# Performance work log

Measured on AMD Instinct MI355X. Metric: run time of the kernel, lower is better.

## Reference

```python
import jax, jax.numpy as jnp
import numpy as np

SS = 25.0 / 255.0   # spatial_scale = 1 / (SEARCH_SIZE/25), SEARCH_SIZE = 255
OUT = 7             # ROIPOOL_OUTSIZE // 4, ROIPOOL_OUTSIZE = 28
SP = 4              # sample_per_part (mmdet DeformRoIPooling default)
TRANS_STD = 0.1


def _deform_roi_pool(x, rois, offset):
    # x: [B,C,H,W]; rois: [N,5] (batch_idx,x1,y1,x2,y2); offset: [N,2,OUT,OUT] (ch0=x, ch1=y)
    B, C, H, W = x.shape
    N = rois.shape[0]
    b = rois[:, 0].astype(jnp.int32)
    sw = jnp.round(rois[:, 1]) * SS - 0.5
    sh = jnp.round(rois[:, 2]) * SS - 0.5
    rw = jnp.maximum((jnp.round(rois[:, 3]) + 1.0) * SS - 0.5 - sw, 0.1)
    rh = jnp.maximum((jnp.round(rois[:, 4]) + 1.0) * SS - 0.5 - sh, 0.1)
    bw, bh = rw / OUT, rh / OUT
    p = jnp.arange(OUT, dtype=x.dtype)
    tx = offset[:, 0] * TRANS_STD  # [N,OUT,OUT] indexed [n,ph,pw]
    ty = offset[:, 1] * TRANS_STD
    wstart = p[None, None, :] * bw[:, None, None] + sw[:, None, None] + tx * rw[:, None, None]
    hstart = p[None, :, None] * bh[:, None, None] + sh[:, None, None] + ty * rh[:, None, None]
    s = jnp.arange(SP, dtype=x.dtype)
    # sample coords [N,OUT,OUT,SP(ih),SP(iw)]
    sx = wstart[..., None, None] + s[None, None, None, None, :] * (bw / SP)[:, None, None, None, None]
    sy = hstart[..., None, None] + s[None, None, None, :, None] * (bh / SP)[:, None, None, None, None]
    valid = (sx >= -0.5) & (sx <= W - 0.5) & (sy >= -0.5) & (sy <= H - 0.5)
    xc = jnp.clip(sx, 0.0, W - 1.0)
    yc = jnp.clip(sy, 0.0, H - 1.0)
    x0 = jnp.floor(xc)
    y0 = jnp.floor(yc)
    dx = xc - x0
    dy = yc - y0
    xi0 = x0.astype(jnp.int32)
    yi0 = y0.astype(jnp.int32)
    xi1 = jnp.ceil(xc).astype(jnp.int32)
    yi1 = jnp.ceil(yc).astype(jnp.int32)
    feat = jnp.transpose(x, (0, 2, 3, 1))  # [B,H,W,C]
    bb = b[:, None, None, None, None]

    def g(yi, xi):
        return feat[bb, yi, xi]  # [N,OUT,OUT,SP,SP,C]

    val = (((1 - dx) * (1 - dy))[..., None] * g(yi0, xi0)
           + (dx * (1 - dy))[..., None] * g(yi0, xi1)
           + ((1 - dx) * dy)[..., None] * g(yi1, xi0)
           + (dx * dy)[..., None] * g(yi1, xi1))
    val = jnp.where(valid[..., None], val, 0.0)
    cnt = valid.sum(axis=(3, 4)).astype(x.dtype)              # [N,OUT,OUT]
    pooled = val.sum(axis=(3, 4)) / jnp.maximum(cnt, 1.0)[..., None]
    return jnp.transpose(pooled, (0, 3, 1, 2))                # [N,C,OUT,OUT]


def _lin(h, w, b):
    return h @ w.T + b


def _forward(x, rois, off_w1, off_b1, off_w2, off_b2, off_w3, off_b3,
             fc1_w, fc1_b, fc2_w, fc2_b, box_w, box_b):
    N = rois.shape[0]
    zero_off = jnp.zeros((N, 2, OUT, OUT), x.dtype)
    # pass 1: no-trans pooling -> offset prediction
    p0 = _deform_roi_pool(x, rois, zero_off).reshape(N, -1)
    h = jax.nn.relu(_lin(p0, off_w1, off_b1))
    h = jax.nn.relu(_lin(h, off_w2, off_b2))
    off = _lin(h, off_w3, off_b3).reshape(N, 2, OUT, OUT)
    # pass 2: deformable pooling with predicted offsets
    p = _deform_roi_pool(x, rois, off).reshape(N, -1)
    h = jax.nn.relu(_lin(p, fc1_w, fc1_b))
    h = jax.nn.relu(_lin(h, fc2_w, fc2_b))
    return _lin(h, box_w, box_b)  # [N,4]


def setup_inputs():
    key = jax.random.key(0)
    ks = jax.random.split(key, 16)
    B, C, H, W, N = 8, 256, 25, 25, 256
    IN = C * OUT * OUT  # 12544
    DFC, FCC = 1024, 512
    x = jax.random.normal(ks[0], (B, C, H, W), jnp.float32)
    bidx = jax.random.randint(ks[1], (N,), 0, B).astype(jnp.float32)
    x1 = jax.random.uniform(ks[2], (N,), minval=0.0, maxval=180.0)
    y1 = jax.random.uniform(ks[3], (N,), minval=0.0, maxval=180.0)
    wd = jax.random.uniform(ks[4], (N,), minval=24.0, maxval=120.0)
    ht = jax.random.uniform(ks[5], (N,), minval=24.0, maxval=120.0)
    rois = jnp.stack([bidx, x1, y1, jnp.clip(x1 + wd, 0.0, 254.0),
                      jnp.clip(y1 + ht, 0.0, 254.0)], axis=1)

    def lin_p(k, o, i):
        return jax.random.normal(k, (o, i), jnp.float32) * (1.0 / np.sqrt(i))

    return dict(
        x=x, rois=rois,
        off_w1=lin_p(ks[6], DFC, IN), off_b1=jnp.zeros((DFC,), jnp.float32),
        off_w2=lin_p(ks[7], DFC, DFC), off_b2=jnp.zeros((DFC,), jnp.float32),
        off_w3=lin_p(ks[8], 2 * OUT * OUT, DFC) * 0.1,
        off_b3=jnp.zeros((2 * OUT * OUT,), jnp.float32),
        fc1_w=lin_p(ks[9], FCC, IN), fc1_b=jnp.zeros((FCC,), jnp.float32),
        fc2_w=lin_p(ks[10], FCC, FCC), fc2_b=jnp.zeros((FCC,), jnp.float32),
        box_w=lin_p(ks[11], 4, FCC) * 0.001, box_b=jnp.zeros((4,), jnp.float32),
    )


def reference(x, rois, off_w1, off_b1, off_w2, off_b2, off_w3, off_b3,
              fc1_w, fc1_b, fc2_w, fc2_b, box_w, box_b):
    return _forward(x, rois, off_w1, off_b1, off_w2, off_b2, off_w3, off_b3,
                    fc1_w, fc1_b, fc2_w, fc2_b, box_w, box_b)
```

## Files before the change

### kernel.cpp

```cpp
#include <hip/hip_runtime.h>
#include <hip/hip_bf16.h>


#define NROI 256
#define NB   8
#define INF  12544
#define DFC  1024
#define FCC  512

typedef __attribute__((ext_vector_type(8))) short short8;
typedef __attribute__((ext_vector_type(4))) float floatx4;

static __device__ __forceinline__ unsigned short f2bf(float f) {
    unsigned int u = __float_as_uint(f);
    unsigned int r = (u + 0x7fffu + ((u >> 16) & 1u)) >> 16;
    return (unsigned short)r;
}

__global__ __launch_bounds__(256) void transpose_kernel(
        const float* __restrict__ x, float* __restrict__ xT) {
    __shared__ float t[32][33];
    int b  = blockIdx.z;
    int cb = blockIdx.y * 32;
    int lb = blockIdx.x * 32;
    int tx = threadIdx.x & 31, ty = threadIdx.x >> 5;
#pragma unroll
    for (int r = 0; r < 4; ++r) {
        int c = cb + ty + r * 8, l = lb + tx;
        if (l < 625) t[ty + r * 8][tx] = x[(size_t)(b * 256 + c) * 625 + l];
    }
    __syncthreads();
#pragma unroll
    for (int r = 0; r < 4; ++r) {
        int l = lb + ty + r * 8, c = cb + tx;
        if (l < 625) xT[((size_t)b * 625 + l) * 256 + c] = t[tx][ty + r * 8];
    }
}

__global__ __launch_bounds__(256) void pool_prep(
        const float* __restrict__ rois, const float* __restrict__ off, int has_off,
        float* __restrict__ wbuf, int* __restrict__ bbuf) {
    __shared__ float g[256][16];
    const float SSC = (float)(25.0 / 255.0);
    int tid = threadIdx.x;
    int idx = blockIdx.x * 256 + tid;
    int n = idx / 49;
    int bin = idx - n * 49;
    const float* r = rois + n * 5;
    int b = (int)r[0];
    float sw = rintf(r[1]) * SSC - 0.5f;
    float sh = rintf(r[2]) * SSC - 0.5f;
    float rw = fmaxf((rintf(r[3]) + 1.0f) * SSC - 0.5f - sw, 0.1f);
    float rh = fmaxf((rintf(r[4]) + 1.0f) * SSC - 0.5f - sh, 0.1f);
    float bw = rw / 7.0f, bh = rh / 7.0f;
    float bws = bw * 0.25f, bhs = bh * 0.25f;
    int ph = bin / 7, pw = bin - ph * 7;
    float tx = 0.f, ty = 0.f;
    if (has_off) {
        tx = off[n * 98 + bin] * 0.1f;
        ty = off[n * 98 + 49 + bin] * 0.1f;
    }
    float wstart = pw * bw + sw + tx * rw;
    float hstart = ph * bh + sh + ty * rh;
#pragma unroll
    for (int i = 0; i < 16; ++i) g[tid][i] = 0.f;
    int gy0 = 0, gx0 = 0, cnt = 0;
#pragma unroll
    for (int s = 0; s < 16; ++s) {
        float fx = wstart + (s & 3) * bws;
        float fy = hstart + (s >> 2) * bhs;
        bool valid = (fx >= -0.5f) && (fx <= 24.5f) && (fy >= -0.5f) && (fy <= 24.5f);
        float xc = fminf(fmaxf(fx, 0.f), 24.f);
        float yc = fminf(fmaxf(fy, 0.f), 24.f);
        float x0f = floorf(xc), y0f = floorf(yc);
        float dx = xc - x0f, dy = yc - y0f;
        int x0 = (int)x0f, y0 = (int)y0f;
        int x1 = (int)ceilf(xc), y1 = (int)ceilf(yc);
        if (s == 0) { gy0 = y0; gx0 = x0; }
        float w00 = (1.f - dx) * (1.f - dy), w01 = dx * (1.f - dy);
        float w10 = (1.f - dx) * dy,         w11 = dx * dy;
        if (!valid) { w00 = w01 = w10 = w11 = 0.f; }
        cnt += valid ? 1 : 0;
        int ry0 = (y0 - gy0) * 4, ry1 = (y1 - gy0) * 4;
        g[tid][ry0 + (x0 - gx0)] += w00;
        g[tid][ry0 + (x1 - gx0)] += w01;
        g[tid][ry1 + (x0 - gx0)] += w10;
        g[tid][ry1 + (x1 - gx0)] += w11;
    }
    float inv = 1.0f / fmaxf((float)cnt, 1.0f);
    float4* wp = (float4*)(wbuf + (size_t)idx * 16);
#pragma unroll
    for (int q = 0; q < 4; ++q)
        wp[q] = make_float4(g[tid][q * 4] * inv, g[tid][q * 4 + 1] * inv,
                            g[tid][q * 4 + 2] * inv, g[tid][q * 4 + 3] * inv);
    bbuf[idx] = gy0 | (gx0 << 8) | (b << 16);
}

__global__ __launch_bounds__(256) void pool_gather(
        const float* __restrict__ feat, const float* __restrict__ wbuf,
        const int* __restrict__ bbuf, unsigned short* __restrict__ P) {
    __shared__ unsigned short sOut[128 * 49];
    int q = blockIdx.x;
    int n = blockIdx.y;
    int tid = threadIdx.x;
    int wv = tid >> 6, lane = tid & 63;
    int cbase = q * 128 + lane * 2;

    for (int bin = wv; bin < 49; bin += 4) {
        int di = n * 49 + bin;
        int base = bbuf[di];
        int gy0 = base & 255, gx0 = (base >> 8) & 255, b = base >> 16;
        const float4* wp = (const float4*)(wbuf + (size_t)di * 16);
        float4 w0 = wp[0], w1 = wp[1], w2 = wp[2], w3 = wp[3];
        float ww[16] = { w0.x, w0.y, w0.z, w0.w, w1.x, w1.y, w1.z, w1.w,
                         w2.x, w2.y, w2.z, w2.w, w3.x, w3.y, w3.z, w3.w };
        int rowOff[4], colOff[4];
#pragma unroll
        for (int r = 0; r < 4; ++r) {
            rowOff[r] = min(gy0 + r, 24) * 25;
            colOff[r] = min(gx0 + r, 24);
        }
        int b625 = b * 625;
        float ax = 0.f, ay = 0.f;
#pragma unroll
        for (int cell = 0; cell < 16; ++cell) {
            int pix = b625 + rowOff[cell >> 2] + colOff[cell & 3];
            float2 v = *(const float2*)(feat + (size_t)pix * 256 + cbase);
            ax += ww[cell] * v.x;
            ay += ww[cell] * v.y;
        }
        sOut[(lane * 2) * 49 + bin] = f2bf(ax);
        sOut[(lane * 2 + 1) * 49 + bin] = f2bf(ay);
    }
    __syncthreads();
    const uint2* so = (const uint2*)sOut;
    uint2* dp = (uint2*)(P + (size_t)n * INF + q * 128 * 49);
    for (int i = tid; i < 128 * 49 / 4; i += 256) dp[i] = so[i];
}

template <int BN>
__global__ __launch_bounds__(256) void gemm_nt_part(
        const unsigned short* __restrict__ A, const float* __restrict__ Bw,
        float* __restrict__ Cpart, int N, int K, int kSteps) {
    constexpr int BM = 256;
    constexpr int LDA = 40;
    __shared__ unsigned short As[BM * LDA];
    __shared__ unsigned short Bs[BN * LDA];
    const int tid = threadIdx.x;
    const int lane = tid & 63;
    const int wave = tid >> 6;
    const int n0 = blockIdx.x * BN;
    const int k0 = blockIdx.z * kSteps * 32;
    const int quad = lane >> 4;
    const int l16 = lane & 15;
    constexpr int FM = 4, FN = BN / 16;
    constexpr int NA = BM * 4 / 256;
    constexpr int NBq = BN * 8 / 256;

    floatx4 acc[FM][FN];
#pragma unroll
    for (int i = 0; i < FM; ++i)
#pragma unroll
        for (int j = 0; j < FN; ++j) acc[i][j] = (floatx4)0.f;

    uint4  ra[NA];
    float4 rb[NBq];
    auto loadTile = [&](int kk) {
#pragma unroll
        for (int i = 0; i < NA; ++i) {
            int idx = tid + i * 256, row = idx >> 2, qq = idx & 3;
            ra[i] = *(const uint4*)(A + (size_t)row * K + kk + qq * 8);
        }
#pragma unroll
        for (int i = 0; i < NBq; ++i) {
            int idx = tid + i * 256, row = idx >> 3, qq = idx & 7;
            rb[i] = *(const float4*)(Bw + (size_t)(n0 + row) * K + kk + qq * 4);
        }
    };

    loadTile(k0);
    for (int ks = 0; ks < kSteps; ++ks) {
#pragma unroll
        for (int i = 0; i < NA; ++i) {
            int idx = tid + i * 256, row = idx >> 2, qq = idx & 3;
            *(uint4*)(As + row * LDA + qq * 8) = ra[i];
        }
#pragma unroll
        for (int i = 0; i < NBq; ++i) {
            int idx = tid + i * 256, row = idx >> 3, qq = idx & 7;
            ushort4 h;
            h.x = f2bf(rb[i].x); h.y = f2bf(rb[i].y);
            h.z = f2bf(rb[i].z); h.w = f2bf(rb[i].w);
            *(ushort4*)(Bs + row * LDA + qq * 4) = h;
        }
        __syncthreads();
        if (ks + 1 < kSteps) loadTile(k0 + (ks + 1) * 32);
        short8 a[FM], bfr[FN];
#pragma unroll
        for (int i = 0; i < FM; ++i)
            a[i] = *(const short8*)(As + (wave * 64 + i * 16 + l16) * LDA + quad * 8);
#pragma unroll
        for (int j = 0; j < FN; ++j)
            bfr[j] = *(const short8*)(Bs + (j * 16 + l16) * LDA + quad * 8);
#pragma unroll
        for (int i = 0; i < FM; ++i)
#pragma unroll
            for (int j = 0; j < FN; ++j)
                acc[i][j] = __builtin_amdgcn_mfma_f32_16x16x32_bf16(a[i], bfr[j], acc[i][j], 0, 0, 0);
        __syncthreads();
    }
    float* Cp = Cpart + (size_t)blockIdx.z * BM * N;
#pragma unroll
    for (int i = 0; i < FM; ++i)
#pragma unroll
        for (int rr = 0; rr < 4; ++rr) {
            int row = wave * 64 + i * 16 + quad * 4 + rr;
            float* cr = Cp + (size_t)row * N + n0;
#pragma unroll
            for (int j = 0; j < FN; ++j)
                cr[j * 16 + l16] = acc[i][j][rr];
        }
}

__global__ __launch_bounds__(256) void reduce_bias(
        const float* __restrict__ part, int zc, int mn4,
        const float* __restrict__ bias, int nmask, int relu,
        unsigned short* __restrict__ obf, float* __restrict__ of) {
    int idx = blockIdx.x * 256 + threadIdx.x;
    if (idx >= mn4) return;
    int idx4 = idx * 4;
    const float* bp = bias + (idx4 & nmask);
    float4 acc = *(const float4*)bp;
    const float4* p = (const float4*)part + idx;
    for (int z = 0; z < zc; ++z) {
        float4 v = p[(size_t)z * mn4];
        acc.x += v.x; acc.y += v.y; acc.z += v.z; acc.w += v.w;
    }
    if (relu) {
        acc.x = fmaxf(acc.x, 0.f); acc.y = fmaxf(acc.y, 0.f);
        acc.z = fmaxf(acc.z, 0.f); acc.w = fmaxf(acc.w, 0.f);
    }
    if (obf) {
        ushort4 h;
        h.x = f2bf(acc.x); h.y = f2bf(acc.y); h.z = f2bf(acc.z); h.w = f2bf(acc.w);
        *(ushort4*)(obf + idx4) = h;
    }
    if (of) *(float4*)(of + idx4) = acc;
}

__global__ __launch_bounds__(128) void fc_small(
        const float* __restrict__ h2, const float* __restrict__ w3,
        const float* __restrict__ b3, float* __restrict__ out) {
    __shared__ float shl[1024];
    int n = blockIdx.x, tid = threadIdx.x;
    for (int i = tid; i < 1024; i += 128) shl[i] = fmaxf(h2[(size_t)n * 1024 + i], 0.f);
    __syncthreads();
    if (tid < 98) {
        float acc = b3[tid];
        const float* w = w3 + (size_t)tid * 1024;
        for (int k = 0; k < 1024; k += 4) {
            float4 wv = *(const float4*)(w + k);
            acc += shl[k] * wv.x + shl[k + 1] * wv.y + shl[k + 2] * wv.z + shl[k + 3] * wv.w;
        }
        out[n * 98 + tid] = acc;
    }
}

__global__ __launch_bounds__(64) void head_kernel(
        const float* __restrict__ h4, const float* __restrict__ bw,
        const float* __restrict__ bb, float* __restrict__ out) {
    int n = blockIdx.x, t = threadIdx.x;
    float a0 = 0, a1 = 0, a2 = 0, a3 = 0;
    for (int k = t; k < 512; k += 64) {
        float v = fmaxf(h4[(size_t)n * 512 + k], 0.f);
        a0 += v * bw[k]; a1 += v * bw[512 + k];
        a2 += v * bw[1024 + k]; a3 += v * bw[1536 + k];
    }
#pragma unroll
    for (int o = 32; o > 0; o >>= 1) {
        a0 += __shfl_down(a0, o); a1 += __shfl_down(a1, o);
        a2 += __shfl_down(a2, o); a3 += __shfl_down(a3, o);
    }
    if (t == 0) {
        out[n * 4 + 0] = a0 + bb[0]; out[n * 4 + 1] = a1 + bb[1];
        out[n * 4 + 2] = a2 + bb[2]; out[n * 4 + 3] = a3 + bb[3];
    }
}

extern "C" void kernel_launch(void* const* d_in, const int* in_sizes, int n_in,
                              void* d_out, int out_size, void* d_ws, size_t ws_size,
                              hipStream_t stream) {
    const float* x      = (const float*)d_in[0];
    const float* rois   = (const float*)d_in[1];
    const float* off_w1 = (const float*)d_in[2];
    const float* off_b1 = (const float*)d_in[3];
    const float* off_w2 = (const float*)d_in[4];
    const float* off_b2 = (const float*)d_in[5];
    const float* off_w3 = (const float*)d_in[6];
    const float* off_b3 = (const float*)d_in[7];
    const float* fc1_w  = (const float*)d_in[8];
    const float* fc1_b  = (const float*)d_in[9];
    const float* fc2_w  = (const float*)d_in[10];
    const float* fc2_b  = (const float*)d_in[11];
    const float* box_w  = (const float*)d_in[12];
    const float* box_b  = (const float*)d_in[13];
    float* out = (float*)d_out;

    char* ws = (char*)d_ws;
    size_t o = 0;
    auto carve = [&](size_t bytes) { char* p = ws + o; o += (bytes + 255) & ~(size_t)255; return p; };
    float*          xT   = (float*)carve((size_t)NB * 625 * 256 * 4);
    unsigned short* P    = (unsigned short*)carve((size_t)NROI * INF * 2);
    unsigned short* h1b  = (unsigned short*)carve((size_t)NROI * DFC * 2);
    float*          h2   = (float*)carve((size_t)NROI * DFC * 4);
    float*          offb = (float*)carve((size_t)NROI * 98 * 4);
    unsigned short* h3b  = (unsigned short*)carve((size_t)NROI * FCC * 2);
    float*          h4   = (float*)carve((size_t)NROI * FCC * 4);
    float*          wbuf = (float*)carve((size_t)NROI * 49 * 16 * 4);
    int*            bbuf = (int*)carve((size_t)NROI * 49 * 4);
    size_t fixed = o;
    const size_t SLAB = (size_t)NROI * DFC * 4;
    int zg1;
    if      (ws_size >= fixed + 28 * SLAB) zg1 = 28;
    else if (ws_size >= fixed + 14 * SLAB) zg1 = 14;
    else                                   zg1 = 7;
    float* part = (float*)carve((size_t)zg1 * SLAB);

    transpose_kernel<<<dim3(20, 8, 8), 256, 0, stream>>>(x, xT);
    pool_prep<<<49, 256, 0, stream>>>(rois, nullptr, 0, wbuf, bbuf);
    pool_gather<<<dim3(2, NROI), 256, 0, stream>>>(xT, wbuf, bbuf, P);
    gemm_nt_part<64><<<dim3(16, 1, zg1), 256, 0, stream>>>(P, off_w1, part, DFC, INF, 392 / zg1);
    reduce_bias<<<256, 256, 0, stream>>>(part, zg1, NROI * DFC / 4, off_b1, DFC - 1, 1, h1b, nullptr);
    gemm_nt_part<64><<<dim3(16, 1, 4), 256, 0, stream>>>(h1b, off_w2, part, DFC, DFC, 8);
    reduce_bias<<<256, 256, 0, stream>>>(part, 4, NROI * DFC / 4, off_b2, DFC - 1, 0, nullptr, h2);
    fc_small<<<NROI, 128, 0, stream>>>(h2, off_w3, off_b3, offb);
    pool_prep<<<49, 256, 0, stream>>>(rois, offb, 1, wbuf, bbuf);
    pool_gather<<<dim3(2, NROI), 256, 0, stream>>>(xT, wbuf, bbuf, P);
    gemm_nt_part<64><<<dim3(8, 1, zg1), 256, 0, stream>>>(P, fc1_w, part, FCC, INF, 392 / zg1);
    reduce_bias<<<128, 256, 0, stream>>>(part, zg1, NROI * FCC / 4, fc1_b, FCC - 1, 1, h3b, nullptr);
    gemm_nt_part<64><<<dim3(8, 1, 4), 256, 0, stream>>>(h3b, fc2_w, part, FCC, FCC, 4);
    reduce_bias<<<128, 256, 0, stream>>>(part, 4, NROI * FCC / 4, fc2_b, FCC - 1, 0, nullptr, h4);
    head_kernel<<<NROI, 64, 0, stream>>>(h4, box_w, box_b, out);
}
```

Before: 339.4 us.

## Load GEMM A tiles straight into LDS with a swizzle, use narrower N tiles

The split-K bf16 GEMM now copies its A tile straight from global memory into LDS with global_load_lds, using an XOR swizzle in place of padding to avoid bank conflicts. The B tile is converted from fp32 and staged one step ahead in registers. The N tile shrinks from 64 to 32, which doubles the grid, and the small GEMMs get more K splits. This aims to cut register staging and VGPR pressure and to raise occupancy, at the cost of more blocks rereading A and a single-buffered LDS that now waits on the async copy at the barrier.

```diff
diff --git a/kernel.cpp b/kernel.cpp
--- a/kernel.cpp
+++ b/kernel.cpp
@@ -15,6 +15,12 @@
     unsigned int u = __float_as_uint(f);
     unsigned int r = (u + 0x7fffu + ((u >> 16) & 1u)) >> 16;
     return (unsigned short)r;
+}
+
+static __device__ __forceinline__ void async_copy16(const void* g, void* l) {
+    __builtin_amdgcn_global_load_lds(
+        (const __attribute__((address_space(1))) unsigned int*)g,
+        (__attribute__((address_space(3))) unsigned int*)l, 16, 0, 0);
 }
 
 __global__ __launch_bounds__(256) void transpose_kernel(
@@ -143,9 +149,9 @@
         const unsigned short* __restrict__ A, const float* __restrict__ Bw,
         float* __restrict__ Cpart, int N, int K, int kSteps) {
     constexpr int BM = 256;
-    constexpr int LDA = 40;
-    __shared__ unsigned short As[BM * LDA];
-    __shared__ unsigned short Bs[BN * LDA];
+    constexpr int LDB = 40;
+    __shared__ unsigned short As[BM * 32];
+    __shared__ unsigned short Bs[BN * LDB];
     const int tid = threadIdx.x;
     const int lane = tid & 63;
     const int wave = tid >> 6;
@@ -154,8 +160,6 @@
     const int quad = lane >> 4;
     const int l16 = lane & 15;
     constexpr int FM = 4, FN = BN / 16;
-    constexpr int NA = BM * 4 / 256;
-    constexpr int NBq = BN * 8 / 256;
 
     floatx4 acc[FM][FN];
 #pragma unroll
@@ -163,51 +167,49 @@
 #pragma unroll
         for (int j = 0; j < FN; ++j) acc[i][j] = (floatx4)0.f;
 
-    uint4  ra[NA];
-    float4 rb[NBq];
-    auto loadTile = [&](int kk) {
-#pragma unroll
-        for (int i = 0; i < NA; ++i) {
-            int idx = tid + i * 256, row = idx >> 2, qq = idx & 3;
-            ra[i] = *(const uint4*)(A + (size_t)row * K + kk + qq * 8);
-        }
-#pragma unroll
-        for (int i = 0; i < NBq; ++i) {
-            int idx = tid + i * 256, row = idx >> 3, qq = idx & 7;
-            rb[i] = *(const float4*)(Bw + (size_t)(n0 + row) * K + kk + qq * 4);
-        }
-    };
-
-    loadTile(k0);
+    const unsigned short* agp[4];
+    void* alp[4];
+#pragma unroll
+    for (int i = 0; i < 4; ++i) {
+        int idx = tid + i * 256;
+        int row = idx >> 2;
+        int qq = (idx & 3) ^ ((row >> 1) & 3);
+        agp[i] = A + (size_t)row * K + qq * 8;
+        alp[i] = (char*)As + ((size_t)i * 256 + wave * 64) * 16;
+    }
+    const int brow = tid >> 3, bq = tid & 7;
+    const float* bgp = Bw + (size_t)(n0 + brow) * K + bq * 4;
+    unsigned short* blp = Bs + brow * LDB + bq * 4;
+
+    float4 bv = *(const float4*)(bgp + k0);
     for (int ks = 0; ks < kSteps; ++ks) {
-#pragma unroll
-        for (int i = 0; i < NA; ++i) {
-            int idx = tid + i * 256, row = idx >> 2, qq = idx & 3;
-            *(uint4*)(As + row * LDA + qq * 8) = ra[i];
-        }
-#pragma unroll
-        for (int i = 0; i < NBq; ++i) {
-            int idx = tid + i * 256, row = idx >> 3, qq = idx & 7;
+        int kk = k0 + ks * 32;
+        __syncthreads();
+#pragma unroll
+        for (int i = 0; i < 4; ++i)
+            async_copy16(agp[i] + kk, alp[i]);
+        {
             ushort4 h;
-            h.x = f2bf(rb[i].x); h.y = f2bf(rb[i].y);
-            h.z = f2bf(rb[i].z); h.w = f2bf(rb[i].w);
-            *(ushort4*)(Bs + row * LDA + qq * 4) = h;
-        }
+            h.x = f2bf(bv.x); h.y = f2bf(bv.y); h.z = f2bf(bv.z); h.w = f2bf(bv.w);
+            *(ushort4*)blp = h;
+        }
+        if (ks + 1 < kSteps) bv = *(const float4*)(bgp + kk + 32);
         __syncthreads();
-        if (ks + 1 < kSteps) loadTile(k0 + (ks + 1) * 32);
         short8 a[FM], bfr[FN];
 #pragma unroll
-        for (int i = 0; i < FM; ++i)
-            a[i] = *(const short8*)(As + (wave * 64 + i * 16 + l16) * LDA + quad * 8);
+        for (int i = 0; i < FM; ++i) {
+            int r = wave * 64 + i * 16 + l16;
+            int slot = quad ^ ((r >> 1) & 3);
+            a[i] = *(const short8*)(As + r * 32 + slot * 8);
+        }
 #pragma unroll
         for (int j = 0; j < FN; ++j)
-            bfr[j] = *(const short8*)(Bs + (j * 16 + l16) * LDA + quad * 8);
+            bfr[j] = *(const short8*)(Bs + (j * 16 + l16) * LDB + quad * 8);
 #pragma unroll
         for (int i = 0; i < FM; ++i)
 #pragma unroll
             for (int j = 0; j < FN; ++j)
                 acc[i][j] = __builtin_amdgcn_mfma_f32_16x16x32_bf16(a[i], bfr[j], acc[i][j], 0, 0, 0);
-        __syncthreads();
     }
     float* Cp = Cpart + (size_t)blockIdx.z * BM * N;
 #pragma unroll
@@ -324,21 +326,22 @@
     if      (ws_size >= fixed + 28 * SLAB) zg1 = 28;
     else if (ws_size >= fixed + 14 * SLAB) zg1 = 14;
     else                                   zg1 = 7;
+    int zg2 = (zg1 >= 8) ? 8 : 4;
     float* part = (float*)carve((size_t)zg1 * SLAB);
 
     transpose_kernel<<<dim3(20, 8, 8), 256, 0, stream>>>(x, xT);
     pool_prep<<<49, 256, 0, stream>>>(rois, nullptr, 0, wbuf, bbuf);
     pool_gather<<<dim3(2, NROI), 256, 0, stream>>>(xT, wbuf, bbuf, P);
-    gemm_nt_part<64><<<dim3(16, 1, zg1), 256, 0, stream>>>(P, off_w1, part, DFC, INF, 392 / zg1);
+    gemm_nt_part<32><<<dim3(32, 1, zg1), 256, 0, stream>>>(P, off_w1, part, DFC, INF, 392 / zg1);
     reduce_bias<<<256, 256, 0, stream>>>(part, zg1, NROI * DFC / 4, off_b1, DFC - 1, 1, h1b, nullptr);
-    gemm_nt_part<64><<<dim3(16, 1, 4), 256, 0, stream>>>(h1b, off_w2, part, DFC, DFC, 8);
-    reduce_bias<<<256, 256, 0, stream>>>(part, 4, NROI * DFC / 4, off_b2, DFC - 1, 0, nullptr, h2);
+    gemm_nt_part<32><<<dim3(32, 1, zg2), 256, 0, stream>>>(h1b, off_w2, part, DFC, DFC, 32 / zg2);
+    reduce_bias<<<256, 256, 0, stream>>>(part, zg2, NROI * DFC / 4, off_b2, DFC - 1, 0, nullptr, h2);
     fc_small<<<NROI, 128, 0, stream>>>(h2, off_w3, off_b3, offb);
     pool_prep<<<49, 256, 0, stream>>>(rois, offb, 1, wbuf, bbuf);
     pool_gather<<<dim3(2, NROI), 256, 0, stream>>>(xT, wbuf, bbuf, P);
-    gemm_nt_part<64><<<dim3(8, 1, zg1), 256, 0, stream>>>(P, fc1_w, part, FCC, INF, 392 / zg1);
+    gemm_nt_part<32><<<dim3(16, 1, zg1), 256, 0, stream>>>(P, fc1_w, part, FCC, INF, 392 / zg1);
     reduce_bias<<<128, 256, 0, stream>>>(part, zg1, NROI * FCC / 4, fc1_b, FCC - 1, 1, h3b, nullptr);
-    gemm_nt_part<64><<<dim3(8, 1, 4), 256, 0, stream>>>(h3b, fc2_w, part, FCC, FCC, 4);
-    reduce_bias<<<128, 256, 0, stream>>>(part, 4, NROI * FCC / 4, fc2_b, FCC - 1, 0, nullptr, h4);
+    gemm_nt_part<32><<<dim3(16, 1, zg2), 256, 0, stream>>>(h3b, fc2_w, part, FCC, FCC, 16 / zg2);
+    reduce_bias<<<128, 256, 0, stream>>>(part, zg2, NROI * FCC / 4, fc2_b, FCC - 1, 0, nullptr, h4);
     head_kernel<<<NROI, 64, 0, stream>>>(h4, box_w, box_b, out);
 }
```

After: 315.5 us. 1.08x faster.
